# Performance work log

Measured on AMD Instinct MI355X. Metric: run time of the kernel, lower is better.

The kernel has to match this reference:

```python
import jax, jax.numpy as jnp
import numpy as np

HEADS = 16
DIM_HEAD = 64
DIM = 1024
SEQ = 2048
BATCH = 1
THR_MIN = 0.01
THR_MAX = 0.9
LN_EPS = 1e-5
NEG = -jnp.finfo(jnp.float32).max


def _ln(x, gamma):
    # torch F.layer_norm over last dim, beta fixed to zeros
    mu = jnp.mean(x, axis=-1, keepdims=True)
    var = jnp.mean(jnp.square(x - mu), axis=-1, keepdims=True)
    return (x - mu) * jax.lax.rsqrt(var + LN_EPS) * gamma


def setup_inputs() -> dict:
    key = jax.random.key(0)
    ks = jax.random.split(key, 8)
    s = 0.02  # realistic init scale for weights
    return {
        "x": jax.random.normal(ks[0], (BATCH, SEQ, DIM), jnp.float32),
        "gamma_norm": jnp.ones((DIM,), jnp.float32),
        "Wq": jax.random.normal(ks[1], (DIM, HEADS * DIM_HEAD), jnp.float32) * s,
        "Wk": jax.random.normal(ks[2], (DIM, HEADS * DIM_HEAD), jnp.float32) * s,
        "Wv": jax.random.normal(ks[3], (DIM, HEADS * DIM_HEAD), jnp.float32) * s,
        "Wout": jax.random.normal(ks[4], (HEADS * DIM_HEAD, DIM), jnp.float32) * s,
        "gamma_out": jnp.ones((DIM,), jnp.float32),
        "W_gcn0": jax.random.normal(ks[5], (DIM_HEAD, DIM_HEAD), jnp.float32) * s,
        "b_gcn0": jnp.zeros((DIM_HEAD,), jnp.float32),
        "W_gcn1": jax.random.normal(ks[6], (DIM_HEAD, DIM_HEAD), jnp.float32) * s,
        "b_gcn1": jnp.zeros((DIM_HEAD,), jnp.float32),
        "W_lin": jax.random.normal(ks[7], (DIM_HEAD, DIM_HEAD), jnp.float32) * s,
        "b_lin": jnp.zeros((DIM_HEAD,), jnp.float32),
    }


def reference(x, gamma_norm, Wq, Wk, Wv, Wout, gamma_out,
              W_gcn0, b_gcn0, W_gcn1, b_gcn1, W_lin, b_lin):
    b, n, _ = x.shape
    h, d = HEADS, DIM_HEAD
    scale = d ** -0.5

    xn = _ln(x, gamma_norm)
    # projections, split heads: b n (h d) -> b h n d
    q = (xn @ Wq).reshape(b, n, h, d).transpose(0, 2, 1, 3) * scale
    k = (xn @ Wk).reshape(b, n, h, d).transpose(0, 2, 1, 3)
    v = (xn @ Wv).reshape(b, n, h, d).transpose(0, 2, 1, 3)

    sim = jnp.einsum("bhid,bhjd->bhij", q, k)
    causal_mask = jnp.triu(jnp.ones((n, n), bool), 1)
    sim = jnp.where(causal_mask, NEG, sim)
    attn = jax.nn.softmax(sim.astype(jnp.float32), axis=-1)  # [b,h,n,n]

    out = jnp.einsum("bhij,bhjd->bhid", attn, v)

    # --- attention-derived adjacency GCN path ---
    adj = attn.reshape(b * h, n, n) + jnp.eye(n, dtype=attn.dtype)
    adj = jnp.clip(adj, 0.0, 1.0)
    adj = jnp.where(adj < THR_MIN, 0.0, adj)
    adj = jnp.where(adj > THR_MAX, 1.0, adj)

    g = v.reshape(b * h, n, d)
    deg = jnp.sum(adj, axis=-1, keepdims=True)  # [bh, n, 1]
    # GCN layer 0 (skip connection, exact GELU like nn.GELU())
    g = jax.nn.gelu(jnp.matmul(adj, g @ W_gcn0 + b_gcn0) / deg + g, approximate=False)
    # GCN layer 1
    g = jax.nn.gelu(jnp.matmul(adj, g @ W_gcn1 + b_gcn1) / deg + g, approximate=False)
    # final linear (dropout inactive in eval)
    g = g @ W_lin + b_lin

    out = out + g.reshape(b, h, n, d)

    # merge heads: b h n d -> b n (h d), output projection + LayerNorm
    out = out.transpose(0, 2, 1, 3).reshape(b, n, h * d)
    out = _ln(out @ Wout, gamma_out)
    return out
```

## Files before the change

kernel.cpp:

```cpp
#include <hip/hip_runtime.h>
#include <hip/hip_bf16.h>
#include <math.h>
#include <stdint.h>

#define DEV __device__ __forceinline__

typedef unsigned short u16;
typedef __attribute__((ext_vector_type(8))) short s16x8;
typedef __attribute__((ext_vector_type(4))) float f32x4;
typedef __attribute__((ext_vector_type(16))) float f32x16;
typedef __attribute__((ext_vector_type(4))) unsigned u32x4;

static constexpr int SEQ = 2048;
static constexpr int DIM = 1024;
static constexpr int HEADS = 16;
static constexpr int QKVLD = 3072;
static constexpr int TOT32 = 2080;

DEV u16 f2bf(float f) {
  unsigned u = __float_as_uint(f);
  u = u + 0x7FFFu + ((u >> 16) & 1u);
  return (u16)(u >> 16);
}
DEV float bf2f(u16 b) { return __uint_as_float(((unsigned)b) << 16); }
DEV float gelu_exact(float x) { return 0.5f * x * (1.0f + erff(x * 0.70710678118654752f)); }

DEV unsigned pkbf(float lo, float hi) {
  __hip_bfloat162 h = __float22bfloat162_rn(make_float2(lo, hi));
  unsigned r; __builtin_memcpy(&r, &h, 4); return r;
}

#define MFMA16(a, b, c) __builtin_amdgcn_mfma_f32_16x16x32_bf16(a, b, c, 0, 0, 0)
#define MFMA32(a, b, c) __builtin_amdgcn_mfma_f32_32x32x16_bf16(a, b, c, 0, 0, 0)

DEV s16x8 u4_to_s8(u32x4 u) { union { u32x4 a; s16x8 b; } c; c.a = u; return c.b; }

DEV void build_frags(const float* p, int hi, s16x8* fr) {
  unsigned pw[4][2];
#pragma unroll
  for (int rq = 0; rq < 4; ++rq) {
    pw[rq][0] = pkbf(p[4 * rq + 0], p[4 * rq + 1]);
    pw[rq][1] = pkbf(p[4 * rq + 2], p[4 * rq + 3]);
  }
#pragma unroll
  for (int m = 0; m < 2; ++m) {
    unsigned x0 = __shfl_xor(pw[2 * m + 1][0], 32);
    unsigned x1 = __shfl_xor(pw[2 * m + 1][1], 32);
    unsigned y0 = __shfl_xor(pw[2 * m][0], 32);
    unsigned y1 = __shfl_xor(pw[2 * m][1], 32);
    u32x4 u;
    u[0] = hi ? x0 : pw[2 * m][0];
    u[1] = hi ? x1 : pw[2 * m][1];
    u[2] = hi ? pw[2 * m + 1][0] : y0;
    u[3] = hi ? pw[2 * m + 1][1] : y1;
    fr[m] = u4_to_s8(u);
  }
}

template<bool OUT_BF16>
__global__ __launch_bounds__(256) void ln_rows(const float* __restrict__ in,
                                               const float* __restrict__ gamma,
                                               void* __restrict__ outp) {
  int row = blockIdx.x;
  const float* x = in + (size_t)row * DIM;
  float v[4];
  float s = 0.f;
#pragma unroll
  for (int e = 0; e < 4; ++e) { v[e] = x[threadIdx.x + 256 * e]; s += v[e]; }
  __shared__ float red[8];
  int lane = threadIdx.x & 63, wid = threadIdx.x >> 6;
#pragma unroll
  for (int off = 32; off; off >>= 1) s += __shfl_xor(s, off);
  if (lane == 0) red[wid] = s;
  __syncthreads();
  float mean = (red[0] + red[1] + red[2] + red[3]) * (1.0f / DIM);
  float vs = 0.f;
#pragma unroll
  for (int e = 0; e < 4; ++e) { float d = v[e] - mean; vs += d * d; }
#pragma unroll
  for (int off = 32; off; off >>= 1) vs += __shfl_xor(vs, off);
  __syncthreads();
  if (lane == 0) red[wid] = vs;
  __syncthreads();
  float var = (red[0] + red[1] + red[2] + red[3]) * (1.0f / DIM);
  float rstd = rsqrtf(var + 1e-5f);
#pragma unroll
  for (int e = 0; e < 4; ++e) {
    int c = threadIdx.x + 256 * e;
    float o = (v[e] - mean) * rstd * gamma[c];
    if (OUT_BF16) ((u16*)outp)[(size_t)row * DIM + c] = f2bf(o);
    else          ((float*)outp)[(size_t)row * DIM + c] = o;
  }
}

__global__ __launch_bounds__(256) void wt_all(
    const float* __restrict__ Wq, const float* __restrict__ Wk, const float* __restrict__ Wv,
    const float* __restrict__ Wout, const float* __restrict__ Wg0,
    const float* __restrict__ Wg1, const float* __restrict__ Wlin,
    u16* __restrict__ WqkvT, u16* __restrict__ WoT,
    u16* __restrict__ Wg0T, u16* __restrict__ Wg1T, u16* __restrict__ WlinT) {
  int z = blockIdx.z;
  const float* src; u16* dst; int R, C, c0, r0;
  if (z < 4) {
    src = (z == 0) ? Wq : (z == 1) ? Wk : (z == 2) ? Wv : Wout;
    dst = (z == 0) ? WqkvT : (z == 1) ? WqkvT + (size_t)DIM * DIM
        : (z == 2) ? WqkvT + (size_t)2 * DIM * DIM : WoT;
    R = DIM; C = DIM; c0 = blockIdx.x * 64; r0 = blockIdx.y * 64;
  } else {
    if (blockIdx.x >= 3 || blockIdx.y > 0) return;
    src = (blockIdx.x == 0) ? Wg0 : (blockIdx.x == 1) ? Wg1 : Wlin;
    dst = (blockIdx.x == 0) ? Wg0T : (blockIdx.x == 1) ? Wg1T : WlinT;
    R = 64; C = 64; c0 = 0; r0 = 0;
  }
  __shared__ float tile[64][65];
  int tx = threadIdx.x & 63, ty = threadIdx.x >> 6;
  for (int rr = ty; rr < 64; rr += 4)
    tile[rr][tx] = src[(size_t)(r0 + rr) * C + c0 + tx];
  __syncthreads();
  for (int rr = ty; rr < 64; rr += 4)
    dst[(size_t)(c0 + rr) * R + r0 + tx] = f2bf(tile[tx][rr]);
}

__global__ __launch_bounds__(256) void pack_qkv(const u16* __restrict__ QKV,
                                                u16* __restrict__ Kp, u16* __restrict__ Vp) {
  int bx = blockIdx.x, h = blockIdx.y;
  int tid = threadIdx.x, wid = tid >> 6, lane = tid & 63;
  int l31 = lane & 31, hi = lane >> 5;
  if (bx < 64) {
    int jb = bx, fi = wid;
    s16x8 v = *(const s16x8*)(QKV + (size_t)(jb * 32 + l31) * QKVLD + 1024 + h * 64 + fi * 16 + hi * 8);
    *(s16x8*)(Kp + ((size_t)(h * 64 + jb) * 4 + fi) * 512 + lane * 8) = v;
  } else {
    int jb16 = bx - 64;
    __shared__ u16 t[16][72];
    if (tid < 128) {
      int r = tid >> 3, c = (tid & 7) * 8;
      *(s16x8*)&t[r][c] = *(const s16x8*)(QKV + (size_t)(jb16 * 16 + r) * QKVLD + 2048 + h * 64 + c);
    }
    __syncthreads();
    if (wid < 2) {
      int dh = wid;
      s16x8 v;
#pragma unroll
      for (int e = 0; e < 8; ++e) v[e] = (short)t[hi * 8 + e][dh * 32 + l31];
      *(s16x8*)(Vp + ((size_t)(h * 128 + jb16) * 2 + dh) * 512 + lane * 8) = v;
    }
  }
}

__global__ __launch_bounds__(256) void gemm_pack(
    const u16* __restrict__ Asrc, int ld, const u16* __restrict__ Wt,
    const float* __restrict__ bias, u16* __restrict__ Hp) {
  int bx = blockIdx.x, h = blockIdx.y;
  __shared__ __align__(16) u16 Ws[64][72];
  __shared__ __align__(16) u16 tt[64][72];
  int tid = threadIdx.x, lane = tid & 63, wid = tid >> 6;
  int l15 = lane & 15, lhi = lane >> 4;
  {
    int r = tid >> 2, cc = (tid & 3) * 8;
    *(s16x8*)&Ws[r][cc] = *(const s16x8*)(Wt + r * 64 + cc);
    *(s16x8*)&Ws[r][cc + 32] = *(const s16x8*)(Wt + r * 64 + cc + 32);
  }
  __syncthreads();
  int j = bx * 64 + wid * 16 + l15;
  const u16* arow = Asrc + (size_t)j * ld + h * 64;
  s16x8 a0 = *(const s16x8*)(arow + lhi * 8);
  s16x8 a1 = *(const s16x8*)(arow + 32 + lhi * 8);
  f32x4 acc[4];
#pragma unroll
  for (int c = 0; c < 4; ++c) {
    acc[c] = f32x4{0.f, 0.f, 0.f, 0.f};
    s16x8 b0 = *(const s16x8*)&Ws[c * 16 + l15][lhi * 8];
    s16x8 b1 = *(const s16x8*)&Ws[c * 16 + l15][32 + lhi * 8];
    acc[c] = MFMA16(a0, b0, acc[c]);
    acc[c] = MFMA16(a1, b1, acc[c]);
  }
  int rl = wid * 16 + lhi * 4;
#pragma unroll
  for (int c = 0; c < 4; ++c)
#pragma unroll
    for (int r = 0; r < 4; ++r)
      tt[rl + r][c * 16 + l15] = f2bf(acc[c][r] + bias[c * 16 + l15]);
  __syncthreads();
  int l31 = lane & 31, hi = lane >> 5;
#pragma unroll
  for (int dh = 0; dh < 2; ++dh) {
    s16x8 v;
#pragma unroll
    for (int e = 0; e < 8; ++e) v[e] = (short)tt[wid * 16 + hi * 8 + e][dh * 32 + l31];
    *(s16x8*)(Hp + ((size_t)(h * 128 + bx * 4 + wid) * 2 + dh) * 512 + lane * 8) = v;
  }
}

DEV void gload_lds16(const u16* g, u16* l) {
  __builtin_amdgcn_global_load_lds(
      (const __attribute__((address_space(1))) unsigned int*)g,
      (__attribute__((address_space(3))) unsigned int*)(unsigned int)(uintptr_t)l,
      16, 0, 0);
}
template<bool OUT_F32>
__global__ __launch_bounds__(256) void gemm128(const u16* __restrict__ A,
                                               const u16* __restrict__ Bt,
                                               void* __restrict__ Cout,
                                               int Nn, int K, int Nq, float qs) {
  __shared__ __align__(16) u16 As[128][64];
  __shared__ __align__(16) u16 Bs[128][64];
  int tid = threadIdx.x, lane = tid & 63, wid = tid >> 6;
  int l15 = lane & 15, lhi = lane >> 4;
  int nwg = gridDim.x * gridDim.y;
  int flat = blockIdx.y * gridDim.x + blockIdx.x;
  int q8 = nwg >> 3, r8 = nwg & 7;
  int xcd = flat & 7, idx = flat >> 3;
  int wg = (xcd < r8) ? xcd * (q8 + 1) + idx : r8 * (q8 + 1) + (xcd - r8) * q8 + idx;
  int bx = wg % gridDim.x, by = wg / gridDim.x;
  int n0 = bx * 128, m0 = by * 128;
  int wr = wid >> 1, wc = wid & 1;
  float scale = (n0 < Nq) ? qs : 1.0f;
  f32x4 acc[4][4];
#pragma unroll
  for (int mi = 0; mi < 4; ++mi)
#pragma unroll
    for (int ni = 0; ni < 4; ++ni) acc[mi][ni] = f32x4{0.f, 0.f, 0.f, 0.f};
  int srow = lane >> 3;
  int scol = ((lane & 7) ^ srow) * 8;
  for (int k0 = 0; k0 < K; k0 += 64) {
    __syncthreads();
#pragma unroll
    for (int i = 0; i < 4; ++i) {
      int row0 = wid * 32 + i * 8;
      gload_lds16(A + (size_t)(m0 + row0 + srow) * K + k0 + scol, &As[row0][0]);
      gload_lds16(Bt + (size_t)(n0 + row0 + srow) * K + k0 + scol, &Bs[row0][0]);
    }
    __syncthreads();
#pragma unroll
    for (int ks = 0; ks < 2; ++ks) {
      s16x8 af[4], bf[4];
#pragma unroll
      for (int mi = 0; mi < 4; ++mi) {
        int row = wr * 64 + mi * 16 + l15;
        int c8 = (ks * 4 + lhi) ^ (row & 7);
        af[mi] = *(const s16x8*)&As[row][c8 * 8];
      }
#pragma unroll
      for (int ni = 0; ni < 4; ++ni) {
        int row = wc * 64 + ni * 16 + l15;
        int c8 = (ks * 4 + lhi) ^ (row & 7);
        bf[ni] = *(const s16x8*)&Bs[row][c8 * 8];
      }
#pragma unroll
      for (int mi = 0; mi < 4; ++mi)
#pragma unroll
        for (int ni = 0; ni < 4; ++ni)
          acc[mi][ni] = MFMA16(af[mi], bf[ni], acc[mi][ni]);
    }
  }
  int orow0 = m0 + wr * 64, ocol0 = n0 + wc * 64;
#pragma unroll
  for (int mi = 0; mi < 4; ++mi)
#pragma unroll
    for (int ni = 0; ni < 4; ++ni)
#pragma unroll
      for (int r = 0; r < 4; ++r) {
        int row = orow0 + mi * 16 + lhi * 4 + r;
        int col = ocol0 + ni * 16 + l15;
        float vv = acc[mi][ni][r] * scale;
        if (OUT_F32) ((float*)Cout)[(size_t)row * Nn + col] = vv;
        else         ((u16*)Cout)[(size_t)row * Nn + col] = f2bf(vv);
      }
}

__global__ __launch_bounds__(256) void small_gemm_add(
    const u16* __restrict__ A, int ldo, const u16* __restrict__ Wt,
    const float* __restrict__ bias, const float* __restrict__ addsrc,
    u16* __restrict__ outp) {
  __shared__ __align__(16) u16 Ws[64][72];
  int tid = threadIdx.x, lane = tid & 63, wid = tid >> 6;
  int l15 = lane & 15, lhi = lane >> 4;
  int m0 = blockIdx.x * 64;
  {
    int r = tid >> 2, cc = (tid & 3) * 8;
    *(s16x8*)&Ws[r][cc] = *(const s16x8*)(Wt + r * 64 + cc);
    *(s16x8*)&Ws[r][cc + 32] = *(const s16x8*)(Wt + r * 64 + cc + 32);
  }
  __syncthreads();
  int R = m0 + wid * 16 + l15;
  const u16* arow = A + (size_t)(R >> 4) * ldo + (R & 15) * 64;
  s16x8 a0 = *(const s16x8*)(arow + lhi * 8);
  s16x8 a1 = *(const s16x8*)(arow + 32 + lhi * 8);
  f32x4 acc[4];
#pragma unroll
  for (int c = 0; c < 4; ++c) {
    acc[c] = f32x4{0.f, 0.f, 0.f, 0.f};
    s16x8 b0 = *(const s16x8*)&Ws[c * 16 + l15][lhi * 8];
    s16x8 b1 = *(const s16x8*)&Ws[c * 16 + l15][32 + lhi * 8];
    acc[c] = MFMA16(a0, b0, acc[c]);
    acc[c] = MFMA16(a1, b1, acc[c]);
  }
  int orow = m0 + wid * 16 + lhi * 4;
#pragma unroll
  for (int c = 0; c < 4; ++c)
#pragma unroll
    for (int r = 0; r < 4; ++r) {
      int col = c * 16 + l15;
      size_t idx = (size_t)(orow + r) * 64 + col;
      outp[idx] = f2bf(acc[c][r] + bias[col] + addsrc[idx]);
    }
}

static constexpr float NEGB = -3.0e38f;
DEV int crowf(int r, int hi) { return (r & 3) + 8 * (r >> 2) + 4 * hi; }

template<bool STORE_ADJ>
__global__ __launch_bounds__(512, 4) void attn_pv(
    const u16* __restrict__ QKV, const u16* __restrict__ Kp, const u16* __restrict__ Vp,
    float* __restrict__ mbuf, float* __restrict__ lbuf, float* __restrict__ degb,
    float* __restrict__ oatt, u16* __restrict__ adjS, unsigned char* __restrict__ maskb) {
  int tid = threadIdx.x, wq = tid >> 6, lane = tid & 63;
  int l31 = lane & 31, hi = lane >> 5;
  int h = blockIdx.x & 15, sidx = blockIdx.x >> 4;
  int s = 63 - sidx;

  __shared__ float cmb[4][2][16][64];
  __shared__ float smf[8][32], slf[8][32], sdg[8][32];

  int qbase = s * 32;
  int cums = (s * (s + 1)) >> 1;
  int n = s + 1;
  int c_lo = (n * wq) >> 3, c_hi = (n * (wq + 1)) >> 3;

  s16x8 qf[4];
#pragma unroll
  for (int fi = 0; fi < 4; ++fi)
    qf[fi] = *(const s16x8*)(QKV + (size_t)(qbase + l31) * QKVLD + h * 64 + fi * 16 + hi * 8);

  float mp = NEGB, lp = 0.f;
  for (int jb = c_lo; jb < c_hi; ++jb) {
    f32x16 sa;
#pragma unroll
    for (int r = 0; r < 16; ++r) sa[r] = 0.f;
#pragma unroll
    for (int fi = 0; fi < 4; ++fi) {
      s16x8 kf = *(const s16x8*)(Kp + ((size_t)(h * 64 + jb) * 4 + fi) * 512 + lane * 8);
      sa = MFMA32(kf, qf[fi], sa);
    }
    bool diag = (jb == s);
    float vmax = NEGB;
#pragma unroll
    for (int r = 0; r < 16; ++r) {
      float v = sa[r];
      if (diag && (crowf(r, hi) > l31)) v = NEGB;
      sa[r] = v; vmax = fmaxf(vmax, v);
    }
    float mn = fmaxf(mp, vmax);
    float es = 0.f;
#pragma unroll
    for (int r = 0; r < 16; ++r) es += __expf(sa[r] - mn);
    lp = lp * __expf(mp - mn) + es;
    mp = mn;
  }
  {
    float mo = __shfl_xor(mp, 32), lo = __shfl_xor(lp, 32);
    float mn = fmaxf(mp, mo);
    lp = lp * __expf(mp - mn) + lo * __expf(mo - mn);
    mp = mn;
  }
  if (hi == 0) { smf[wq][l31] = mp; slf[wq][l31] = lp; }
  __syncthreads();
  float mt = NEGB, lt = 0.f;
#pragma unroll
  for (int w2 = 0; w2 < 8; ++w2) {
    float mo = smf[w2][l31], lo = slf[w2][l31];
    float mn = fmaxf(mt, mo);
    lt = lt * __expf(mt - mn) + lo * __expf(mo - mn);
    mt = mn;
  }
  float invl = 1.0f / lt;
  if (wq == 0 && hi == 0) {
    mbuf[(size_t)h * SEQ + qbase + l31] = mt;
    lbuf[(size_t)h * SEQ + qbase + l31] = lt;
  }

  f32x16 pv0, pv1;
#pragma unroll
  for (int r = 0; r < 16; ++r) { pv0[r] = 0.f; pv1[r] = 0.f; }
  float dacc = 0.f;
  for (int jb = c_lo; jb < c_hi; ++jb) {
    f32x16 sa;
#pragma unroll
    for (int r = 0; r < 16; ++r) sa[r] = 0.f;
#pragma unroll
    for (int fi = 0; fi < 4; ++fi) {
      s16x8 kf = *(const s16x8*)(Kp + ((size_t)(h * 64 + jb) * 4 + fi) * 512 + lane * 8);
      sa = MFMA32(kf, qf[fi], sa);
    }
    bool diag = (jb == s);
    float p[16];
#pragma unroll
    for (int r = 0; r < 16; ++r) {
      bool valid = !diag || (crowf(r, hi) <= l31);
      p[r] = valid ? __expf(sa[r] - mt) * invl : 0.f;
    }
    s16x8 pf[2]; build_frags(p, hi, pf);
#pragma unroll
    for (int m = 0; m < 2; ++m) {
      const u16* vb = Vp + ((size_t)(h * 128 + jb * 2 + m) * 2) * 512;
      pv0 = MFMA32(pf[m], *(const s16x8*)(vb + lane * 8), pv0);
      pv1 = MFMA32(pf[m], *(const s16x8*)(vb + 512 + lane * 8), pv1);
    }
    float as0 = 0.f, as1 = 0.f;
#pragma unroll
    for (int r = 0; r < 16; ++r) {
      float pp = p[r];
      float a = (diag && (crowf(r, hi) == l31)) ? 1.f
                : ((pp < 0.01f) ? 0.f : ((pp > 0.9f) ? 1.f : pp));
      p[r] = a; dacc += a;
      if (r < 8) as0 += a; else as1 += a;
    }
    unsigned flags = (__ballot(as0 > 0.f) ? 1u : 0u) | (__ballot(as1 > 0.f) ? 2u : 0u);
    if (STORE_ADJ && flags) {
      s16x8 af[2]; build_frags(p, hi, af);
      size_t fb = ((size_t)h * TOT32 + cums + jb) * 2;
#pragma unroll
      for (int m = 0; m < 2; ++m) if ((flags >> m) & 1u)
        *(s16x8*)(adjS + (fb + m) * 512 + lane * 8) = af[m];
    }
    if (lane == 0) maskb[(size_t)h * TOT32 + cums + jb] = (unsigned char)flags;
  }
  dacc += __shfl_xor(dacc, 32);
  if (hi == 0) sdg[wq][l31] = dacc;
  if (wq >= 4) {
#pragma unroll
    for (int r = 0; r < 16; ++r) {
      cmb[wq - 4][0][r][lane] = pv0[r];
      cmb[wq - 4][1][r][lane] = pv1[r];
    }
  }
  __syncthreads();
  if (wq < 4) {
#pragma unroll
    for (int r = 0; r < 16; ++r) {
      pv0[r] += cmb[wq][0][r][lane];
      pv1[r] += cmb[wq][1][r][lane];
    }
  }
  __syncthreads();
  if (wq == 2 || wq == 3) {
#pragma unroll
    for (int r = 0; r < 16; ++r) {
      cmb[wq - 2][0][r][lane] = pv0[r];
      cmb[wq - 2][1][r][lane] = pv1[r];
    }
  }
  __syncthreads();
  if (wq < 2) {
#pragma unroll
    for (int r = 0; r < 16; ++r) {
      pv0[r] += cmb[wq][0][r][lane];
      pv1[r] += cmb[wq][1][r][lane];
    }
  }
  __syncthreads();
  if (wq == 1) {
#pragma unroll
    for (int r = 0; r < 16; ++r) {
      cmb[0][0][r][lane] = pv0[r];
      cmb[0][1][r][lane] = pv1[r];
    }
  }
  __syncthreads();
  if (wq == 0) {
    if (hi == 0) {
      float dt = 0.f;
#pragma unroll
      for (int w2 = 0; w2 < 8; ++w2) dt += sdg[w2][l31];
      degb[(size_t)h * SEQ + qbase + l31] = dt;
    }
#pragma unroll
    for (int r = 0; r < 16; ++r) {
      pv0[r] += cmb[0][0][r][lane];
      pv1[r] += cmb[0][1][r][lane];
    }
#pragma unroll
    for (int r = 0; r < 16; ++r) {
      int qr = qbase + crowf(r, hi);
      oatt[(size_t)qr * DIM + h * 64 + l31] = pv0[r];
      oatt[(size_t)qr * DIM + h * 64 + 32 + l31] = pv1[r];
    }
  }
}

template<bool READ_ADJ>
__global__ __launch_bounds__(512, 4) void gcn_apply(
    const u16* __restrict__ QKV, const u16* __restrict__ Kp,
    const u16* __restrict__ Hp, const u16* __restrict__ adjS,
    const unsigned char* __restrict__ maskb,
    const float* __restrict__ mbuf, const float* __restrict__ lbuf,
    const float* __restrict__ degb,
    const u16* __restrict__ skip, int skipld, u16* __restrict__ outp) {
  int tid = threadIdx.x, wq = tid >> 6, lane = tid & 63;
  int l31 = lane & 31, hi = lane >> 5;
  int h = blockIdx.x & 15, sidx = blockIdx.x >> 4;
  int s = 63 - sidx;

  __shared__ float cmb[4][2][16][64];

  int qbase = s * 32;
  int cums = (s * (s + 1)) >> 1;
  int n = s + 1;
  int c_lo = (n * wq) >> 3, c_hi = (n * (wq + 1)) >> 3;

  f32x16 gc0, gc1;
#pragma unroll
  for (int r = 0; r < 16; ++r) { gc0[r] = 0.f; gc1[r] = 0.f; }

  if constexpr (READ_ADJ) {
    for (int jb = c_lo; jb < c_hi; ++jb) {
      unsigned flags = maskb[(size_t)h * TOT32 + cums + jb];
      if (!flags) continue;
      size_t fb = ((size_t)h * TOT32 + cums + jb) * 2;
#pragma unroll
      for (int m = 0; m < 2; ++m) if ((flags >> m) & 1u) {
        s16x8 af = *(const s16x8*)(adjS + (fb + m) * 512 + lane * 8);
        const u16* hb = Hp + ((size_t)(h * 128 + jb * 2 + m) * 2) * 512;
        gc0 = MFMA32(af, *(const s16x8*)(hb + lane * 8), gc0);
        gc1 = MFMA32(af, *(const s16x8*)(hb + 512 + lane * 8), gc1);
      }
    }
  } else {
    s16x8 qf[4];
#pragma unroll
    for (int fi = 0; fi < 4; ++fi)
      qf[fi] = *(const s16x8*)(QKV + (size_t)(qbase + l31) * QKVLD + h * 64 + fi * 16 + hi * 8);
    float mt = mbuf[(size_t)h * SEQ + qbase + l31];
    float invl = 1.0f / lbuf[(size_t)h * SEQ + qbase + l31];
    for (int jb = c_lo; jb < c_hi; ++jb) {
      unsigned flags = maskb[(size_t)h * TOT32 + cums + jb];
      if (!flags) continue;
      f32x16 sa;
#pragma unroll
      for (int r = 0; r < 16; ++r) sa[r] = 0.f;
#pragma unroll
      for (int fi = 0; fi < 4; ++fi) {
        s16x8 kf = *(const s16x8*)(Kp + ((size_t)(h * 64 + jb) * 4 + fi) * 512 + lane * 8);
        sa = MFMA32(kf, qf[fi], sa);
      }
      bool diag = (jb == s);
      float p[16];
#pragma unroll
      for (int r = 0; r < 16; ++r) {
        int cr = crowf(r, hi);
        bool valid = !diag || (cr <= l31);
        float pp = valid ? __expf(sa[r] - mt) * invl : 0.f;
        p[r] = (diag && (cr == l31)) ? 1.f
               : ((pp < 0.01f) ? 0.f : ((pp > 0.9f) ? 1.f : pp));
      }
      s16x8 af[2]; build_frags(p, hi, af);
#pragma unroll
      for (int m = 0; m < 2; ++m) if ((flags >> m) & 1u) {
        const u16* hb = Hp + ((size_t)(h * 128 + jb * 2 + m) * 2) * 512;
        gc0 = MFMA32(af[m], *(const s16x8*)(hb + lane * 8), gc0);
        gc1 = MFMA32(af[m], *(const s16x8*)(hb + 512 + lane * 8), gc1);
      }
    }
  }

  if (wq >= 4) {
#pragma unroll
    for (int r = 0; r < 16; ++r) {
      cmb[wq - 4][0][r][lane] = gc0[r];
      cmb[wq - 4][1][r][lane] = gc1[r];
    }
  }
  __syncthreads();
  if (wq < 4) {
#pragma unroll
    for (int r = 0; r < 16; ++r) {
      gc0[r] += cmb[wq][0][r][lane];
      gc1[r] += cmb[wq][1][r][lane];
    }
  }
  __syncthreads();
  if (wq == 2 || wq == 3) {
#pragma unroll
    for (int r = 0; r < 16; ++r) {
      cmb[wq - 2][0][r][lane] = gc0[r];
      cmb[wq - 2][1][r][lane] = gc1[r];
    }
  }
  __syncthreads();
  if (wq < 2) {
#pragma unroll
    for (int r = 0; r < 16; ++r) {
      gc0[r] += cmb[wq][0][r][lane];
      gc1[r] += cmb[wq][1][r][lane];
    }
  }
  __syncthreads();
  if (wq == 1) {
#pragma unroll
    for (int r = 0; r < 16; ++r) {
      cmb[0][0][r][lane] = gc0[r];
      cmb[0][1][r][lane] = gc1[r];
    }
  }
  __syncthreads();
  if (wq == 0) {
#pragma unroll
    for (int r = 0; r < 16; ++r) {
      gc0[r] += cmb[0][0][r][lane];
      gc1[r] += cmb[0][1][r][lane];
    }
#pragma unroll
    for (int r = 0; r < 16; ++r) {
      int qr = qbase + crowf(r, hi);
      float dinv = 1.0f / degb[(size_t)h * SEQ + qr];
      float sk0 = bf2f(skip[(size_t)qr * skipld + h * 64 + l31]);
      float sk1 = bf2f(skip[(size_t)qr * skipld + h * 64 + 32 + l31]);
      outp[(size_t)qr * DIM + h * 64 + l31] = f2bf(gelu_exact(gc0[r] * dinv + sk0));
      outp[(size_t)qr * DIM + h * 64 + 32 + l31] = f2bf(gelu_exact(gc1[r] * dinv + sk1));
    }
  }
}

extern "C" void kernel_launch(void* const* d_in, const int* in_sizes, int n_in,
                              void* d_out, int out_size, void* d_ws, size_t ws_size,
                              hipStream_t stream) {
  (void)in_sizes; (void)n_in; (void)out_size;
  const float* x       = (const float*)d_in[0];
  const float* gamma_n = (const float*)d_in[1];
  const float* Wq      = (const float*)d_in[2];
  const float* Wk      = (const float*)d_in[3];
  const float* Wv      = (const float*)d_in[4];
  const float* Wout    = (const float*)d_in[5];
  const float* gamma_o = (const float*)d_in[6];
  const float* Wg0     = (const float*)d_in[7];
  const float* bg0     = (const float*)d_in[8];
  const float* Wg1     = (const float*)d_in[9];
  const float* bg1     = (const float*)d_in[10];
  const float* Wlin    = (const float*)d_in[11];
  const float* blin    = (const float*)d_in[12];
  float* out = (float*)d_out;

  char* w = (char*)d_ws;
  size_t off = 0;
  auto alloc = [&](size_t bytes) -> void* {
    void* p = w + off;
    off = (off + bytes + 255) & ~(size_t)255;
    return p;
  };
  u16* xn      = (u16*)alloc((size_t)SEQ * DIM * 2);
  u16* WqkvT   = (u16*)alloc((size_t)3 * DIM * DIM * 2);
  u16* WoT     = (u16*)alloc((size_t)DIM * DIM * 2);
  u16* Wg0T    = (u16*)alloc(64 * 64 * 2);
  u16* Wg1T    = (u16*)alloc(64 * 64 * 2);
  u16* WlinT   = (u16*)alloc(64 * 64 * 2);
  u16* QKV     = (u16*)alloc((size_t)SEQ * QKVLD * 2);
  float* mbuf  = (float*)alloc((size_t)HEADS * SEQ * 4);
  float* lbuf  = (float*)alloc((size_t)HEADS * SEQ * 4);
  float* degb  = (float*)alloc((size_t)HEADS * SEQ * 4);
  float* oatt  = (float*)alloc((size_t)SEQ * DIM * 4);
  u16* g1      = (u16*)alloc((size_t)SEQ * DIM * 2);
  u16* g2      = (u16*)alloc((size_t)SEQ * DIM * 2);
  u16* Kp      = (u16*)alloc((size_t)HEADS * 64 * 4 * 512 * 2);
  u16* Vp      = (u16*)alloc((size_t)HEADS * 128 * 2 * 512 * 2);
  u16* H0p     = (u16*)alloc((size_t)HEADS * 128 * 2 * 512 * 2);
  u16* H1p     = (u16*)alloc((size_t)HEADS * 128 * 2 * 512 * 2);
  u16* Om      = (u16*)alloc((size_t)SEQ * DIM * 2);
  unsigned char* maskb = (unsigned char*)alloc((size_t)HEADS * TOT32);
  float* Y     = (float*)QKV;

  size_t adj_bytes = (size_t)HEADS * TOT32 * 2 * 512 * 2;
  bool use_adj = (off + adj_bytes) <= ws_size;
  u16* adjS = use_adj ? (u16*)alloc(adj_bytes) : nullptr;

  ln_rows<true><<<SEQ, 256, 0, stream>>>(x, gamma_n, xn);
  wt_all<<<dim3(16, 16, 5), 256, 0, stream>>>(Wq, Wk, Wv, Wout, Wg0, Wg1, Wlin,
                                              WqkvT, WoT, Wg0T, Wg1T, WlinT);
  gemm128<false><<<dim3(24, 16), 256, 0, stream>>>(xn, WqkvT, QKV, QKVLD, DIM, 1024, 0.125f);
  pack_qkv<<<dim3(192, 16), 256, 0, stream>>>(QKV, Kp, Vp);
  gemm_pack<<<dim3(32, 16), 256, 0, stream>>>(QKV + 2048, QKVLD, Wg0T, bg0, H0p);
  if (use_adj)
    attn_pv<true><<<1024, 512, 0, stream>>>(QKV, Kp, Vp, mbuf, lbuf, degb, oatt, adjS, maskb);
  else
    attn_pv<false><<<1024, 512, 0, stream>>>(QKV, Kp, Vp, mbuf, lbuf, degb, oatt, nullptr, maskb);
  if (use_adj)
    gcn_apply<true><<<1024, 512, 0, stream>>>(QKV, Kp, H0p, adjS, maskb, mbuf, lbuf, degb,
                                              QKV + 2048, QKVLD, g1);
  else
    gcn_apply<false><<<1024, 512, 0, stream>>>(QKV, Kp, H0p, nullptr, maskb, mbuf, lbuf, degb,
                                               QKV + 2048, QKVLD, g1);
  gemm_pack<<<dim3(32, 16), 256, 0, stream>>>(g1, DIM, Wg1T, bg1, H1p);
  if (use_adj)
    gcn_apply<true><<<1024, 512, 0, stream>>>(QKV, Kp, H1p, adjS, maskb, mbuf, lbuf, degb,
                                              g1, DIM, g2);
  else
    gcn_apply<false><<<1024, 512, 0, stream>>>(QKV, Kp, H1p, nullptr, maskb, mbuf, lbuf, degb,
                                               g1, DIM, g2);
  small_gemm_add<<<512, 256, 0, stream>>>(g2, DIM, WlinT, blin, oatt, Om);
  gemm128<true><<<dim3(8, 16), 256, 0, stream>>>(Om, WoT, Y, DIM, DIM, 0, 1.0f);
  ln_rows<false><<<SEQ, 256, 0, stream>>>(Y, gamma_o, out);
}
```

Baseline: 150.9 us.

## Fold log2e into Q scale, shrink GEMM tiles, bf16 thresholding, setprio

Templates the GEMM on tile sizes and launches smaller tiles for the QKV and output projections so more workgroups are in flight. Folds log2(e) into the Q scale so softmax can use exp2f instead of expf. Adds s_setprio around MFMA sections and computes adjacency thresholds directly on bf16 fragment bits, dropping a second fragment build. Degree sums now come from bf16-rounded values, which slightly changes numerics.

Result: faster. 144.6 us (-4.2%).

```diff
diff --git a/kernel.cpp b/kernel.cpp
--- a/kernel.cpp
+++ b/kernel.cpp
@@ -16,6 +16,7 @@
 static constexpr int HEADS = 16;
 static constexpr int QKVLD = 3072;
 static constexpr int TOT32 = 2080;
+static constexpr float LOG2E = 1.4426950408889634f;
 
 DEV u16 f2bf(float f) {
   unsigned u = __float_as_uint(f);
@@ -198,13 +199,15 @@
       (__attribute__((address_space(3))) unsigned int*)(unsigned int)(uintptr_t)l,
       16, 0, 0);
 }
-template<bool OUT_F32>
-__global__ __launch_bounds__(256) void gemm128(const u16* __restrict__ A,
-                                               const u16* __restrict__ Bt,
-                                               void* __restrict__ Cout,
-                                               int Nn, int K, int Nq, float qs) {
-  __shared__ __align__(16) u16 As[128][64];
-  __shared__ __align__(16) u16 Bs[128][64];
+template<int BM, int BN, bool OUT_F32>
+__global__ __launch_bounds__(256) void gemm_t(const u16* __restrict__ A,
+                                              const u16* __restrict__ Bt,
+                                              void* __restrict__ Cout,
+                                              int Nn, int K, int Nq, float qs) {
+  constexpr int MI = BM / 32;
+  constexpr int NI = BN / 32;
+  __shared__ __align__(16) u16 As[BM][64];
+  __shared__ __align__(16) u16 Bs[BN][64];
   int tid = threadIdx.x, lane = tid & 63, wid = tid >> 6;
   int l15 = lane & 15, lhi = lane >> 4;
   int nwg = gridDim.x * gridDim.y;
@@ -213,52 +216,56 @@
   int xcd = flat & 7, idx = flat >> 3;
   int wg = (xcd < r8) ? xcd * (q8 + 1) + idx : r8 * (q8 + 1) + (xcd - r8) * q8 + idx;
   int bx = wg % gridDim.x, by = wg / gridDim.x;
-  int n0 = bx * 128, m0 = by * 128;
+  int n0 = bx * BN, m0 = by * BM;
   int wr = wid >> 1, wc = wid & 1;
   float scale = (n0 < Nq) ? qs : 1.0f;
-  f32x4 acc[4][4];
-#pragma unroll
-  for (int mi = 0; mi < 4; ++mi)
-#pragma unroll
-    for (int ni = 0; ni < 4; ++ni) acc[mi][ni] = f32x4{0.f, 0.f, 0.f, 0.f};
+  f32x4 acc[MI][NI];
+#pragma unroll
+  for (int mi = 0; mi < MI; ++mi)
+#pragma unroll
+    for (int ni = 0; ni < NI; ++ni) acc[mi][ni] = f32x4{0.f, 0.f, 0.f, 0.f};
   int srow = lane >> 3;
   int scol = ((lane & 7) ^ srow) * 8;
   for (int k0 = 0; k0 < K; k0 += 64) {
     __syncthreads();
 #pragma unroll
-    for (int i = 0; i < 4; ++i) {
-      int row0 = wid * 32 + i * 8;
+    for (int i = 0; i < BM / 32; ++i) {
+      int row0 = (wid * (BM / 32) + i) * 8;
       gload_lds16(A + (size_t)(m0 + row0 + srow) * K + k0 + scol, &As[row0][0]);
+    }
+#pragma unroll
+    for (int i = 0; i < BN / 32; ++i) {
+      int row0 = (wid * (BN / 32) + i) * 8;
       gload_lds16(Bt + (size_t)(n0 + row0 + srow) * K + k0 + scol, &Bs[row0][0]);
     }
     __syncthreads();
 #pragma unroll
     for (int ks = 0; ks < 2; ++ks) {
-      s16x8 af[4], bf[4];
-#pragma unroll
-      for (int mi = 0; mi < 4; ++mi) {
-        int row = wr * 64 + mi * 16 + l15;
+      s16x8 af[MI], bf[NI];
+#pragma unroll
+      for (int mi = 0; mi < MI; ++mi) {
+        int row = wr * (BM / 2) + mi * 16 + l15;
         int c8 = (ks * 4 + lhi) ^ (row & 7);
         af[mi] = *(const s16x8*)&As[row][c8 * 8];
       }
 #pragma unroll
-      for (int ni = 0; ni < 4; ++ni) {
-        int row = wc * 64 + ni * 16 + l15;
+      for (int ni = 0; ni < NI; ++ni) {
+        int row = wc * (BN / 2) + ni * 16 + l15;
         int c8 = (ks * 4 + lhi) ^ (row & 7);
         bf[ni] = *(const s16x8*)&Bs[row][c8 * 8];
       }
 #pragma unroll
-      for (int mi = 0; mi < 4; ++mi)
-#pragma unroll
-        for (int ni = 0; ni < 4; ++ni)
+      for (int mi = 0; mi < MI; ++mi)
+#pragma unroll
+        for (int ni = 0; ni < NI; ++ni)
           acc[mi][ni] = MFMA16(af[mi], bf[ni], acc[mi][ni]);
     }
   }
-  int orow0 = m0 + wr * 64, ocol0 = n0 + wc * 64;
-#pragma unroll
-  for (int mi = 0; mi < 4; ++mi)
-#pragma unroll
-    for (int ni = 0; ni < 4; ++ni)
+  int orow0 = m0 + wr * (BM / 2), ocol0 = n0 + wc * (BN / 2);
+#pragma unroll
+  for (int mi = 0; mi < MI; ++mi)
+#pragma unroll
+    for (int ni = 0; ni < NI; ++ni)
 #pragma unroll
       for (int r = 0; r < 4; ++r) {
         int row = orow0 + mi * 16 + lhi * 4 + r;
@@ -338,11 +345,13 @@
     f32x16 sa;
 #pragma unroll
     for (int r = 0; r < 16; ++r) sa[r] = 0.f;
+    __builtin_amdgcn_s_setprio(1);
 #pragma unroll
     for (int fi = 0; fi < 4; ++fi) {
       s16x8 kf = *(const s16x8*)(Kp + ((size_t)(h * 64 + jb) * 4 + fi) * 512 + lane * 8);
       sa = MFMA32(kf, qf[fi], sa);
     }
+    __builtin_amdgcn_s_setprio(0);
     bool diag = (jb == s);
     float vmax = NEGB;
 #pragma unroll
@@ -354,14 +363,14 @@
     float mn = fmaxf(mp, vmax);
     float es = 0.f;
 #pragma unroll
-    for (int r = 0; r < 16; ++r) es += __expf(sa[r] - mn);
-    lp = lp * __expf(mp - mn) + es;
+    for (int r = 0; r < 16; ++r) es += exp2f(sa[r] - mn);
+    lp = lp * exp2f(mp - mn) + es;
     mp = mn;
   }
   {
     float mo = __shfl_xor(mp, 32), lo = __shfl_xor(lp, 32);
     float mn = fmaxf(mp, mo);
-    lp = lp * __expf(mp - mn) + lo * __expf(mo - mn);
+    lp = lp * exp2f(mp - mn) + lo * exp2f(mo - mn);
     mp = mn;
   }
   if (hi == 0) { smf[wq][l31] = mp; slf[wq][l31] = lp; }
@@ -371,7 +380,7 @@
   for (int w2 = 0; w2 < 8; ++w2) {
     float mo = smf[w2][l31], lo = slf[w2][l31];
     float mn = fmaxf(mt, mo);
-    lt = lt * __expf(mt - mn) + lo * __expf(mo - mn);
+    lt = lt * exp2f(mt - mn) + lo * exp2f(mo - mn);
     mt = mn;
   }
   float invl = 1.0f / lt;
@@ -388,37 +397,57 @@
     f32x16 sa;
 #pragma unroll
     for (int r = 0; r < 16; ++r) sa[r] = 0.f;
+    __builtin_amdgcn_s_setprio(1);
 #pragma unroll
     for (int fi = 0; fi < 4; ++fi) {
       s16x8 kf = *(const s16x8*)(Kp + ((size_t)(h * 64 + jb) * 4 + fi) * 512 + lane * 8);
       sa = MFMA32(kf, qf[fi], sa);
     }
+    __builtin_amdgcn_s_setprio(0);
     bool diag = (jb == s);
     float p[16];
 #pragma unroll
     for (int r = 0; r < 16; ++r) {
       bool valid = !diag || (crowf(r, hi) <= l31);
-      p[r] = valid ? __expf(sa[r] - mt) * invl : 0.f;
+      p[r] = valid ? exp2f(sa[r] - mt) * invl : 0.f;
     }
     s16x8 pf[2]; build_frags(p, hi, pf);
+    __builtin_amdgcn_s_setprio(1);
 #pragma unroll
     for (int m = 0; m < 2; ++m) {
       const u16* vb = Vp + ((size_t)(h * 128 + jb * 2 + m) * 2) * 512;
       pv0 = MFMA32(pf[m], *(const s16x8*)(vb + lane * 8), pv0);
       pv1 = MFMA32(pf[m], *(const s16x8*)(vb + 512 + lane * 8), pv1);
     }
-    float as0 = 0.f, as1 = 0.f;
-#pragma unroll
-    for (int r = 0; r < 16; ++r) {
-      float pp = p[r];
-      float a = (diag && (crowf(r, hi) == l31)) ? 1.f
-                : ((pp < 0.01f) ? 0.f : ((pp > 0.9f) ? 1.f : pp));
-      p[r] = a; dacc += a;
-      if (r < 8) as0 += a; else as1 += a;
-    }
-    unsigned flags = (__ballot(as0 > 0.f) ? 1u : 0u) | (__ballot(as1 > 0.f) ? 2u : 0u);
+    __builtin_amdgcn_s_setprio(0);
+    s16x8 af[2];
+#pragma unroll
+    for (int m = 0; m < 2; ++m) {
+      s16x8 a = pf[m];
+#pragma unroll
+      for (int e = 0; e < 8; ++e) {
+        u16 v = (u16)a[e];
+        u16 t = (v < (u16)0x3C24) ? (u16)0 : ((v > (u16)0x3F66) ? (u16)0x3F80 : v);
+        a[e] = (short)t;
+      }
+      af[m] = a;
+    }
+    if (diag) {
+#pragma unroll
+      for (int m = 0; m < 2; ++m)
+#pragma unroll
+        for (int e = 0; e < 8; ++e)
+          if (l31 == m * 16 + hi * 8 + e) af[m][e] = (short)0x3F80;
+    }
+    float asum0 = 0.f, asum1 = 0.f;
+#pragma unroll
+    for (int e = 0; e < 8; ++e) {
+      asum0 += bf2f((u16)af[0][e]);
+      asum1 += bf2f((u16)af[1][e]);
+    }
+    dacc += asum0 + asum1;
+    unsigned flags = (__ballot(asum0 > 0.f) ? 1u : 0u) | (__ballot(asum1 > 0.f) ? 2u : 0u);
     if (STORE_ADJ && flags) {
-      s16x8 af[2]; build_frags(p, hi, af);
       size_t fb = ((size_t)h * TOT32 + cums + jb) * 2;
 #pragma unroll
       for (int m = 0; m < 2; ++m) if ((flags >> m) & 1u)
@@ -550,7 +579,7 @@
       for (int r = 0; r < 16; ++r) {
         int cr = crowf(r, hi);
         bool valid = !diag || (cr <= l31);
-        float pp = valid ? __expf(sa[r] - mt) * invl : 0.f;
+        float pp = valid ? exp2f(sa[r] - mt) * invl : 0.f;
         p[r] = (diag && (cr == l31)) ? 1.f
                : ((pp < 0.01f) ? 0.f : ((pp > 0.9f) ? 1.f : pp));
       }
@@ -676,7 +705,8 @@
   ln_rows<true><<<SEQ, 256, 0, stream>>>(x, gamma_n, xn);
   wt_all<<<dim3(16, 16, 5), 256, 0, stream>>>(Wq, Wk, Wv, Wout, Wg0, Wg1, Wlin,
                                               WqkvT, WoT, Wg0T, Wg1T, WlinT);
-  gemm128<false><<<dim3(24, 16), 256, 0, stream>>>(xn, WqkvT, QKV, QKVLD, DIM, 1024, 0.125f);
+  gemm_t<64, 128, false><<<dim3(24, 32), 256, 0, stream>>>(xn, WqkvT, QKV, QKVLD, DIM,
+                                                           1024, 0.125f * LOG2E);
   pack_qkv<<<dim3(192, 16), 256, 0, stream>>>(QKV, Kp, Vp);
   gemm_pack<<<dim3(32, 16), 256, 0, stream>>>(QKV + 2048, QKVLD, Wg0T, bg0, H0p);
   if (use_adj)
@@ -697,6 +727,6 @@
     gcn_apply<false><<<1024, 512, 0, stream>>>(QKV, Kp, H1p, nullptr, maskb, mbuf, lbuf, degb,
                                                g1, DIM, g2);
   small_gemm_add<<<512, 256, 0, stream>>>(g2, DIM, WlinT, blin, oatt, Om);
-  gemm128<true><<<dim3(8, 16), 256, 0, stream>>>(Om, WoT, Y, DIM, DIM, 0, 1.0f);
+  gemm_t<64, 64, true><<<dim3(16, 32), 256, 0, stream>>>(Om, WoT, Y, DIM, DIM, 0, 1.0f);
   ln_rows<false><<<SEQ, 256, 0, stream>>>(Y, gamma_o, out);
 }
```
